# Kernel tuning notes

Measured on AMD Instinct MI355X. Metric: run time of the kernel, lower is better.

## Reference

```python
import jax, jax.numpy as jnp
import numpy as np

NCLS, NDF, B = 256, 512, 1024
ALP = 0.1


def setup_inputs() -> dict:
    key = jax.random.key(0)
    k1, k2, k3 = jax.random.split(key, 3)
    df = jax.random.normal(k1, (B, NDF), dtype=jnp.float32)
    gt = jax.random.randint(k2, (B,), 0, NCLS)
    fc = jax.random.normal(k3, (NCLS, NDF), dtype=jnp.float32)
    return {"df": df, "gt": gt, "fc": fc}


def _update_stats(df, gt):
    """Sequential per-sample running mean/var update (moving_avg=False branch).
    Faithful to the torch no_grad loop: per-class counter `it`, c1=it/(it+1),
    c2=1/(it+1); mean[t]=f when it==0 else mean[t]*c1+f*c2;
    var[t]=var[t]*c1 + (f-mean[t])**2 * c1*c2. Buffers start at zero.
    """
    mean0 = jnp.zeros((NCLS, NDF), jnp.float32)
    var0 = jnp.zeros((NCLS, NDF), jnp.float32)
    it0 = jnp.zeros((NCLS,), jnp.int32)

    def step(carry, xt):
        mean, var, it = carry
        f, t = xt
        n = it[t]
        nf = n.astype(jnp.float32)
        c1 = nf / (nf + 1.0)
        c2 = 1.0 / (nf + 1.0)
        m_t = jnp.where(n == 0, f, mean[t] * c1 + f * c2)
        a = (f - m_t) ** 2
        v_t = var[t] * c1 + a * c1 * c2
        return (mean.at[t].set(m_t), var.at[t].set(v_t), it.at[t].add(1)), None

    (mean, var, it), _ = jax.lax.scan(step, (mean0, var0, it0), (df, gt))
    return mean, var


def reference(df, gt, fc):
    # stats updated from detached features (torch uses no_grad)
    _, var = _update_stats(jax.lax.stop_gradient(df), gt)
    Var = var[gt]          # (B, ndf)
    Fc = fc[gt]            # (B, ndf): column of fc for each sample's class
    W = fc[None, :, :] - Fc[:, None, :]  # (B, ncls, ndf)
    # score[b,c] = W[b,c,:].df[b,:] + alp/2 * (W**2)[b,c,:].Var[b,:]
    score = jnp.einsum('bcd,bd->bc', W, df) \
        + 0.5 * ALP * jnp.einsum('bcd,bd->bc', W * W, Var)
    return score[:, :, None]  # (B, ncls, 1), matching torch matmul output
```

## Files before the change

kernel.cpp:

```cpp
#include <hip/hip_runtime.h>

#define NCLS 256
#define NDF  512
#define BSZ  1024
#define ALP  0.1f


typedef __attribute__((ext_vector_type(8))) short bf16x8;
typedef __attribute__((ext_vector_type(4))) float f32x4;

__device__ __forceinline__ unsigned rne_pk(float lo, float hi) {
    union { float f; unsigned u; } a, b;
    a.f = lo; b.f = hi;
    unsigned ua = (a.u + 0x7FFFu + ((a.u >> 16) & 1u)) >> 16;
    unsigned ub = (b.u + 0x7FFFu + ((b.u >> 16) & 1u)) & 0xFFFF0000u;
    return ua | ub;
}
__device__ __forceinline__ uint4 pk16(float4 p, float4 q) {
    uint4 r;
    r.x = rne_pk(p.x, p.y); r.y = rne_pk(p.z, p.w);
    r.z = rne_pk(q.x, q.y); r.w = rne_pk(q.z, q.w);
    return r;
}

__global__ __launch_bounds__(256) void fused_main(const float* __restrict__ df,
                                                  const int* __restrict__ gt,
                                                  const float* __restrict__ fc,
                                                  float* __restrict__ s1p,
                                                  float* __restrict__ Rp) {
    __shared__ union {
        struct { alignas(16) char A[64 * 128]; alignas(16) char B[64 * 128]; } g;
        struct { int gts[BSZ]; unsigned long long bmap[64 * 16]; } r;
    } sm;

    const int tid = threadIdx.x;
    const int bid = blockIdx.x;
    const int lane = tid & 63;
    const int wv = tid >> 6;
    const int wm = (wv >> 1) * 32, wn = (wv & 1) * 32;
    const int fr = lane & 15;
    const int fkb = (lane >> 4) * 16;
    const int fswz = (fr & 7) << 4;

    const int sr = tid >> 2;
    const int skb = (tid & 3) * 32;
    const int sswz = (sr & 7) << 4;

    f32x4 acc[2][2];
    acc[0][0] = 0.f; acc[0][1] = 0.f; acc[1][0] = 0.f; acc[1][1] = 0.f;

    auto mma_step = [&](int k0b) {
        const int kb = (k0b + fkb) ^ fswz;
        const bf16x8 aF0 = *(const bf16x8*)(sm.g.A + (wm + fr) * 128 + kb);
        const bf16x8 aF1 = *(const bf16x8*)(sm.g.A + (wm + 16 + fr) * 128 + kb);
        const bf16x8 bF0 = *(const bf16x8*)(sm.g.B + (wn + fr) * 128 + kb);
        const bf16x8 bF1 = *(const bf16x8*)(sm.g.B + (wn + 16 + fr) * 128 + kb);
        acc[0][0] = __builtin_amdgcn_mfma_f32_16x16x32_bf16(aF0, bF0, acc[0][0], 0, 0, 0);
        acc[0][1] = __builtin_amdgcn_mfma_f32_16x16x32_bf16(aF0, bF1, acc[0][1], 0, 0, 0);
        acc[1][0] = __builtin_amdgcn_mfma_f32_16x16x32_bf16(aF1, bF0, acc[1][0], 0, 0, 0);
        acc[1][1] = __builtin_amdgcn_mfma_f32_16x16x32_bf16(aF1, bF1, acc[1][1], 0, 0, 0);
    };
    auto store_tile = [&](float* base) {
#pragma unroll
        for (int mi = 0; mi < 2; ++mi)
#pragma unroll
            for (int ni = 0; ni < 2; ++ni)
#pragma unroll
                for (int r2 = 0; r2 < 4; ++r2)
                    base[(wm + mi * 16 + (lane >> 4) * 4 + r2) * NCLS + wn + ni * 16 + fr] =
                        acc[mi][ni][r2];
    };

    char* arow = sm.g.A + sr * 128;
    char* brow = sm.g.B + sr * 128;

    if (bid >= 128) {
        const int sid = bid - 128;
        const int z = sid & 7;
        const int tile = sid >> 3;
        const int bm = tile & 15, bn = tile >> 4;
        const float* Ag = df + (bm * 64 + sr) * NDF + z * 64 + (tid & 3) * 16;
        const float* Bg = fc + (bn * 64 + sr) * NDF + z * 64 + (tid & 3) * 16;

        const float4 a0 = ((const float4*)Ag)[0], a1 = ((const float4*)Ag)[1],
                     a2 = ((const float4*)Ag)[2], a3 = ((const float4*)Ag)[3];
        const float4 b0 = ((const float4*)Bg)[0], b1 = ((const float4*)Bg)[1],
                     b2 = ((const float4*)Bg)[2], b3 = ((const float4*)Bg)[3];
        *(uint4*)(arow + (skb ^ sswz)) = pk16(a0, a1);
        *(uint4*)(arow + ((skb + 16) ^ sswz)) = pk16(a2, a3);
        *(uint4*)(brow + (skb ^ sswz)) = pk16(b0, b1);
        *(uint4*)(brow + ((skb + 16) ^ sswz)) = pk16(b2, b3);
        __syncthreads();
        mma_step(0); mma_step(64);
        store_tile(s1p + z * (BSZ * NCLS) + (bm * 64) * NCLS + bn * 64);
    } else {
        const int z = bid & 7;
        const int tile = bid >> 3;
        const int bm = tile & 3, bn = tile >> 2;
        const int D0 = z * 64;
        const int clocal = sr;
        const int dg = tid & 3;
        const int myclass = bm * 64 + clocal;
        const int dim0 = D0 + dg * 16;

        const float* Bg = fc + (bn * 64 + sr) * NDF + D0 + (tid & 3) * 16;
        const float4 b0 = ((const float4*)Bg)[0], b1 = ((const float4*)Bg)[1],
                     b2 = ((const float4*)Bg)[2], b3 = ((const float4*)Bg)[3];

        for (int i = tid; i < BSZ; i += 256) sm.r.gts[i] = gt[i];
        for (int i = tid; i < 1024; i += 256) sm.r.bmap[i] = 0ull;
        __syncthreads();
        for (int i = tid; i < BSZ; i += 256) {
            const int c = sm.r.gts[i] - bm * 64;
            if ((unsigned)c < 64u) atomicOr(&sm.r.bmap[c * 16 + (i >> 6)], 1ull << (i & 63));
        }
        const float* fct = fc + myclass * NDF + dim0;
        float fcq[16];
        {
            const float4 q0 = ((const float4*)fct)[0], q1 = ((const float4*)fct)[1];
            const float4 q2 = ((const float4*)fct)[2], q3 = ((const float4*)fct)[3];
            fcq[0]=q0.x; fcq[1]=q0.y; fcq[2]=q0.z; fcq[3]=q0.w;
            fcq[4]=q1.x; fcq[5]=q1.y; fcq[6]=q1.z; fcq[7]=q1.w;
            fcq[8]=q2.x; fcq[9]=q2.y; fcq[10]=q2.z; fcq[11]=q2.w;
            fcq[12]=q3.x; fcq[13]=q3.y; fcq[14]=q3.z; fcq[15]=q3.w;
        }
        __syncthreads();

        float m[16], v[16];
#pragma unroll
        for (int j = 0; j < 16; ++j) { m[j] = 0.f; v[j] = 0.f; }
        float nf = 0.f;
        {
            int w = 0;
            unsigned long long bits = sm.r.bmap[clocal * 16];
            auto next = [&]() -> int {
                while (bits == 0ull) {
                    if (w >= 15) return -1;
                    bits = sm.r.bmap[clocal * 16 + (++w)];
                }
                const int b = __ffsll((unsigned long long)bits) - 1;
                bits &= bits - 1ull;
                return (w << 6) + b;
            };
            int cur = next();
            float f[16];
            if (cur >= 0) {
                const float* p = df + cur * NDF + dim0;
                const float4 q0 = ((const float4*)p)[0], q1 = ((const float4*)p)[1];
                const float4 q2 = ((const float4*)p)[2], q3 = ((const float4*)p)[3];
                f[0]=q0.x; f[1]=q0.y; f[2]=q0.z; f[3]=q0.w;
                f[4]=q1.x; f[5]=q1.y; f[6]=q1.z; f[7]=q1.w;
                f[8]=q2.x; f[9]=q2.y; f[10]=q2.z; f[11]=q2.w;
                f[12]=q3.x; f[13]=q3.y; f[14]=q3.z; f[15]=q3.w;
            }
            while (cur >= 0) {
                const int nxt = next();
                float g[16];
                if (nxt >= 0) {
                    const float* p = df + nxt * NDF + dim0;
                    const float4 q0 = ((const float4*)p)[0], q1 = ((const float4*)p)[1];
                    const float4 q2 = ((const float4*)p)[2], q3 = ((const float4*)p)[3];
                    g[0]=q0.x; g[1]=q0.y; g[2]=q0.z; g[3]=q0.w;
                    g[4]=q1.x; g[5]=q1.y; g[6]=q1.z; g[7]=q1.w;
                    g[8]=q2.x; g[9]=q2.y; g[10]=q2.z; g[11]=q2.w;
                    g[12]=q3.x; g[13]=q3.y; g[14]=q3.z; g[15]=q3.w;
                }
                const float c2 = 1.0f / (nf + 1.0f);
                const float c1 = nf * c2;
                const float c12 = c1 * c2;
#pragma unroll
                for (int j = 0; j < 16; ++j) {
                    m[j] = m[j] * c1 + f[j] * c2;
                    const float a = f[j] - m[j];
                    v[j] = v[j] * c1 + a * a * c12;
                }
                nf += 1.0f;
#pragma unroll
                for (int j = 0; j < 16; ++j) f[j] = g[j];
                cur = nxt;
            }
        }
        __syncthreads();

        {
            float4 p0, p1, p2, p3;
            p0.x=-2.f*fcq[0]*v[0];  p0.y=-2.f*fcq[1]*v[1];  p0.z=-2.f*fcq[2]*v[2];  p0.w=-2.f*fcq[3]*v[3];
            p1.x=-2.f*fcq[4]*v[4];  p1.y=-2.f*fcq[5]*v[5];  p1.z=-2.f*fcq[6]*v[6];  p1.w=-2.f*fcq[7]*v[7];
            p2.x=-2.f*fcq[8]*v[8];  p2.y=-2.f*fcq[9]*v[9];  p2.z=-2.f*fcq[10]*v[10]; p2.w=-2.f*fcq[11]*v[11];
            p3.x=-2.f*fcq[12]*v[12]; p3.y=-2.f*fcq[13]*v[13]; p3.z=-2.f*fcq[14]*v[14]; p3.w=-2.f*fcq[15]*v[15];
            *(uint4*)(arow + (skb ^ sswz)) = pk16(p0, p1);
            *(uint4*)(arow + ((skb + 16) ^ sswz)) = pk16(p2, p3);
            *(uint4*)(brow + (skb ^ sswz)) = pk16(b0, b1);
            *(uint4*)(brow + ((skb + 16) ^ sswz)) = pk16(b2, b3);
        }
        __syncthreads();
        mma_step(0); mma_step(64);
        __syncthreads();
        {
            float4 p0, p1, p2, p3, s0, s1, s2, s3;
            p0.x=v[0];  p0.y=v[1];  p0.z=v[2];  p0.w=v[3];
            p1.x=v[4];  p1.y=v[5];  p1.z=v[6];  p1.w=v[7];
            p2.x=v[8];  p2.y=v[9];  p2.z=v[10]; p2.w=v[11];
            p3.x=v[12]; p3.y=v[13]; p3.z=v[14]; p3.w=v[15];
            s0.x=b0.x*b0.x; s0.y=b0.y*b0.y; s0.z=b0.z*b0.z; s0.w=b0.w*b0.w;
            s1.x=b1.x*b1.x; s1.y=b1.y*b1.y; s1.z=b1.z*b1.z; s1.w=b1.w*b1.w;
            s2.x=b2.x*b2.x; s2.y=b2.y*b2.y; s2.z=b2.z*b2.z; s2.w=b2.w*b2.w;
            s3.x=b3.x*b3.x; s3.y=b3.y*b3.y; s3.z=b3.z*b3.z; s3.w=b3.w*b3.w;
            *(uint4*)(arow + (skb ^ sswz)) = pk16(p0, p1);
            *(uint4*)(arow + ((skb + 16) ^ sswz)) = pk16(p2, p3);
            *(uint4*)(brow + (skb ^ sswz)) = pk16(s0, s1);
            *(uint4*)(brow + ((skb + 16) ^ sswz)) = pk16(s2, s3);
        }
        __syncthreads();
        mma_step(0); mma_step(64);
        store_tile(Rp + z * (NCLS * NCLS) + (bm * 64) * NCLS + bn * 64);
    }
}

__global__ __launch_bounds__(256) void epilogue_kernel(const float* __restrict__ s1p,
                                                       const float* __restrict__ Rp,
                                                       const int* __restrict__ gt,
                                                       float* __restrict__ out) {
    const int b = blockIdx.x * 4 + (threadIdx.x >> 6);
    const int cq = (threadIdx.x & 63) * 4;
    const int t = gt[b];
    float4 v1 = make_float4(0.f, 0.f, 0.f, 0.f);
    float v1t = 0.f;
#pragma unroll
    for (int zz = 0; zz < 8; ++zz) {
        const float* row = s1p + zz * (BSZ * NCLS) + b * NCLS;
        const float4 q = *(const float4*)(row + cq);
        v1.x += q.x; v1.y += q.y; v1.z += q.z; v1.w += q.w;
        v1t += row[t];
    }
    float4 vR = make_float4(0.f, 0.f, 0.f, 0.f);
    float vRt = 0.f;
#pragma unroll
    for (int zz = 0; zz < 8; ++zz) {
        const float* row = Rp + zz * (NCLS * NCLS) + t * NCLS;
        const float4 q = *(const float4*)(row + cq);
        vR.x += q.x; vR.y += q.y; vR.z += q.z; vR.w += q.w;
        vRt += row[t];
    }
    float4 o;
    o.x = (v1.x - v1t) + 0.5f * ALP * (vR.x - vRt);
    o.y = (v1.y - v1t) + 0.5f * ALP * (vR.y - vRt);
    o.z = (v1.z - v1t) + 0.5f * ALP * (vR.z - vRt);
    o.w = (v1.w - v1t) + 0.5f * ALP * (vR.w - vRt);
    *(float4*)(out + b * NCLS + cq) = o;
}

extern "C" void kernel_launch(void* const* d_in, const int* in_sizes, int n_in,
                              void* d_out, int out_size, void* d_ws, size_t ws_size,
                              hipStream_t stream) {
    const float* df = (const float*)d_in[0];
    const int* gt = (const int*)d_in[1];
    const float* fc = (const float*)d_in[2];
    float* out = (float*)d_out;

    float* ws = (float*)d_ws;
    float* s1p = ws;
    float* Rp = s1p + 8 * BSZ * NCLS;

    fused_main<<<640, 256, 0, stream>>>(df, gt, fc, s1p, Rp);
    epilogue_kernel<<<256, 256, 0, stream>>>(s1p, Rp, gt, out);
}
```

Measured before the change: 27.25 us.

## Halve split-K partials for GEMM blocks and fuse the two R-path MFMAs into one K=128 pass

The df·fc GEMM blocks now cover 128 of K each instead of 64, giving 4 split-K slices instead of 8. That halves the s1 partial buffers the epilogue writes and reads, and drops the launch from 640 to 384 blocks. In the stats/R blocks, the two chained MFMA passes (-2·fc·var times fc, and var times fc²) are concatenated along K into one 256-byte-wide shared tile, removing a sync and a reload round. The cost is more registers per thread, double the shared memory, and fewer blocks for latency hiding.

```diff
diff --git a/kernel.cpp b/kernel.cpp
--- a/kernel.cpp
+++ b/kernel.cpp
@@ -29,7 +29,7 @@
                                                   float* __restrict__ s1p,
                                                   float* __restrict__ Rp) {
     __shared__ union {
-        struct { alignas(16) char A[64 * 128]; alignas(16) char B[64 * 128]; } g;
+        struct { alignas(16) char A[64 * 256]; alignas(16) char B[64 * 256]; } g;
         struct { int gts[BSZ]; unsigned long long bmap[64 * 16]; } r;
     } sm;
 
@@ -43,18 +43,19 @@
     const int fswz = (fr & 7) << 4;
 
     const int sr = tid >> 2;
-    const int skb = (tid & 3) * 32;
     const int sswz = (sr & 7) << 4;
+    char* arow = sm.g.A + sr * 256;
+    char* brow = sm.g.B + sr * 256;
 
     f32x4 acc[2][2];
     acc[0][0] = 0.f; acc[0][1] = 0.f; acc[1][0] = 0.f; acc[1][1] = 0.f;
 
     auto mma_step = [&](int k0b) {
         const int kb = (k0b + fkb) ^ fswz;
-        const bf16x8 aF0 = *(const bf16x8*)(sm.g.A + (wm + fr) * 128 + kb);
-        const bf16x8 aF1 = *(const bf16x8*)(sm.g.A + (wm + 16 + fr) * 128 + kb);
-        const bf16x8 bF0 = *(const bf16x8*)(sm.g.B + (wn + fr) * 128 + kb);
-        const bf16x8 bF1 = *(const bf16x8*)(sm.g.B + (wn + 16 + fr) * 128 + kb);
+        const bf16x8 aF0 = *(const bf16x8*)(sm.g.A + (wm + fr) * 256 + kb);
+        const bf16x8 aF1 = *(const bf16x8*)(sm.g.A + (wm + 16 + fr) * 256 + kb);
+        const bf16x8 bF0 = *(const bf16x8*)(sm.g.B + (wn + fr) * 256 + kb);
+        const bf16x8 bF1 = *(const bf16x8*)(sm.g.B + (wn + 16 + fr) * 256 + kb);
         acc[0][0] = __builtin_amdgcn_mfma_f32_16x16x32_bf16(aF0, bF0, acc[0][0], 0, 0, 0);
         acc[0][1] = __builtin_amdgcn_mfma_f32_16x16x32_bf16(aF0, bF1, acc[0][1], 0, 0, 0);
         acc[1][0] = __builtin_amdgcn_mfma_f32_16x16x32_bf16(aF1, bF0, acc[1][0], 0, 0, 0);
@@ -71,27 +72,30 @@
                         acc[mi][ni][r2];
     };
 
-    char* arow = sm.g.A + sr * 128;
-    char* brow = sm.g.B + sr * 128;
-
     if (bid >= 128) {
         const int sid = bid - 128;
-        const int z = sid & 7;
-        const int tile = sid >> 3;
+        const int z = sid & 3;
+        const int tile = sid >> 2;
         const int bm = tile & 15, bn = tile >> 4;
-        const float* Ag = df + (bm * 64 + sr) * NDF + z * 64 + (tid & 3) * 16;
-        const float* Bg = fc + (bn * 64 + sr) * NDF + z * 64 + (tid & 3) * 16;
-
-        const float4 a0 = ((const float4*)Ag)[0], a1 = ((const float4*)Ag)[1],
-                     a2 = ((const float4*)Ag)[2], a3 = ((const float4*)Ag)[3];
-        const float4 b0 = ((const float4*)Bg)[0], b1 = ((const float4*)Bg)[1],
-                     b2 = ((const float4*)Bg)[2], b3 = ((const float4*)Bg)[3];
-        *(uint4*)(arow + (skb ^ sswz)) = pk16(a0, a1);
-        *(uint4*)(arow + ((skb + 16) ^ sswz)) = pk16(a2, a3);
-        *(uint4*)(brow + (skb ^ sswz)) = pk16(b0, b1);
-        *(uint4*)(brow + ((skb + 16) ^ sswz)) = pk16(b2, b3);
-        __syncthreads();
-        mma_step(0); mma_step(64);
+        const float* Ag = df + (bm * 64 + sr) * NDF + z * 128 + (tid & 3) * 32;
+        const float* Bg = fc + (bn * 64 + sr) * NDF + z * 128 + (tid & 3) * 32;
+        const int kbase = (tid & 3) * 64;
+
+        float4 a[8], b[8];
+#pragma unroll
+        for (int i = 0; i < 8; ++i) a[i] = ((const float4*)Ag)[i];
+#pragma unroll
+        for (int i = 0; i < 8; ++i) b[i] = ((const float4*)Bg)[i];
+        *(uint4*)(arow + ((kbase + 0) ^ sswz)) = pk16(a[0], a[1]);
+        *(uint4*)(arow + ((kbase + 16) ^ sswz)) = pk16(a[2], a[3]);
+        *(uint4*)(arow + ((kbase + 32) ^ sswz)) = pk16(a[4], a[5]);
+        *(uint4*)(arow + ((kbase + 48) ^ sswz)) = pk16(a[6], a[7]);
+        *(uint4*)(brow + ((kbase + 0) ^ sswz)) = pk16(b[0], b[1]);
+        *(uint4*)(brow + ((kbase + 16) ^ sswz)) = pk16(b[2], b[3]);
+        *(uint4*)(brow + ((kbase + 32) ^ sswz)) = pk16(b[4], b[5]);
+        *(uint4*)(brow + ((kbase + 48) ^ sswz)) = pk16(b[6], b[7]);
+        __syncthreads();
+        mma_step(0); mma_step(64); mma_step(128); mma_step(192);
         store_tile(s1p + z * (BSZ * NCLS) + (bm * 64) * NCLS + bn * 64);
     } else {
         const int z = bid & 7;
@@ -99,11 +103,12 @@
         const int bm = tile & 3, bn = tile >> 2;
         const int D0 = z * 64;
         const int clocal = sr;
-        const int dg = tid & 3;
         const int myclass = bm * 64 + clocal;
-        const int dim0 = D0 + dg * 16;
-
-        const float* Bg = fc + (bn * 64 + sr) * NDF + D0 + (tid & 3) * 16;
+        const int dim0 = D0 + (tid & 3) * 16;
+        const int kbl = (tid & 3) * 32;
+        const int kbq = 128 + kbl;
+
+        const float* Bg = fc + (bn * 64 + sr) * NDF + dim0;
         const float4 b0 = ((const float4*)Bg)[0], b1 = ((const float4*)Bg)[1],
                      b2 = ((const float4*)Bg)[2], b3 = ((const float4*)Bg)[3];
 
@@ -183,36 +188,32 @@
         __syncthreads();
 
         {
+            float4 l0, l1, l2, l3;
+            l0.x=-2.f*fcq[0]*v[0];  l0.y=-2.f*fcq[1]*v[1];  l0.z=-2.f*fcq[2]*v[2];  l0.w=-2.f*fcq[3]*v[3];
+            l1.x=-2.f*fcq[4]*v[4];  l1.y=-2.f*fcq[5]*v[5];  l1.z=-2.f*fcq[6]*v[6];  l1.w=-2.f*fcq[7]*v[7];
+            l2.x=-2.f*fcq[8]*v[8];  l2.y=-2.f*fcq[9]*v[9];  l2.z=-2.f*fcq[10]*v[10]; l2.w=-2.f*fcq[11]*v[11];
+            l3.x=-2.f*fcq[12]*v[12]; l3.y=-2.f*fcq[13]*v[13]; l3.z=-2.f*fcq[14]*v[14]; l3.w=-2.f*fcq[15]*v[15];
             float4 p0, p1, p2, p3;
-            p0.x=-2.f*fcq[0]*v[0];  p0.y=-2.f*fcq[1]*v[1];  p0.z=-2.f*fcq[2]*v[2];  p0.w=-2.f*fcq[3]*v[3];
-            p1.x=-2.f*fcq[4]*v[4];  p1.y=-2.f*fcq[5]*v[5];  p1.z=-2.f*fcq[6]*v[6];  p1.w=-2.f*fcq[7]*v[7];
-            p2.x=-2.f*fcq[8]*v[8];  p2.y=-2.f*fcq[9]*v[9];  p2.z=-2.f*fcq[10]*v[10]; p2.w=-2.f*fcq[11]*v[11];
-            p3.x=-2.f*fcq[12]*v[12]; p3.y=-2.f*fcq[13]*v[13]; p3.z=-2.f*fcq[14]*v[14]; p3.w=-2.f*fcq[15]*v[15];
-            *(uint4*)(arow + (skb ^ sswz)) = pk16(p0, p1);
-            *(uint4*)(arow + ((skb + 16) ^ sswz)) = pk16(p2, p3);
-            *(uint4*)(brow + (skb ^ sswz)) = pk16(b0, b1);
-            *(uint4*)(brow + ((skb + 16) ^ sswz)) = pk16(b2, b3);
-        }
-        __syncthreads();
-        mma_step(0); mma_step(64);
-        __syncthreads();
-        {
-            float4 p0, p1, p2, p3, s0, s1, s2, s3;
             p0.x=v[0];  p0.y=v[1];  p0.z=v[2];  p0.w=v[3];
             p1.x=v[4];  p1.y=v[5];  p1.z=v[6];  p1.w=v[7];
             p2.x=v[8];  p2.y=v[9];  p2.z=v[10]; p2.w=v[11];
             p3.x=v[12]; p3.y=v[13]; p3.z=v[14]; p3.w=v[15];
+            float4 s0, s1, s2, s3;
             s0.x=b0.x*b0.x; s0.y=b0.y*b0.y; s0.z=b0.z*b0.z; s0.w=b0.w*b0.w;
             s1.x=b1.x*b1.x; s1.y=b1.y*b1.y; s1.z=b1.z*b1.z; s1.w=b1.w*b1.w;
             s2.x=b2.x*b2.x; s2.y=b2.y*b2.y; s2.z=b2.z*b2.z; s2.w=b2.w*b2.w;
             s3.x=b3.x*b3.x; s3.y=b3.y*b3.y; s3.z=b3.z*b3.z; s3.w=b3.w*b3.w;
-            *(uint4*)(arow + (skb ^ sswz)) = pk16(p0, p1);
-            *(uint4*)(arow + ((skb + 16) ^ sswz)) = pk16(p2, p3);
-            *(uint4*)(brow + (skb ^ sswz)) = pk16(s0, s1);
-            *(uint4*)(brow + ((skb + 16) ^ sswz)) = pk16(s2, s3);
-        }
-        __syncthreads();
-        mma_step(0); mma_step(64);
+            *(uint4*)(arow + ((kbl + 0) ^ sswz)) = pk16(l0, l1);
+            *(uint4*)(arow + ((kbl + 16) ^ sswz)) = pk16(l2, l3);
+            *(uint4*)(arow + ((kbq + 0) ^ sswz)) = pk16(p0, p1);
+            *(uint4*)(arow + ((kbq + 16) ^ sswz)) = pk16(p2, p3);
+            *(uint4*)(brow + ((kbl + 0) ^ sswz)) = pk16(b0, b1);
+            *(uint4*)(brow + ((kbl + 16) ^ sswz)) = pk16(b2, b3);
+            *(uint4*)(brow + ((kbq + 0) ^ sswz)) = pk16(s0, s1);
+            *(uint4*)(brow + ((kbq + 16) ^ sswz)) = pk16(s2, s3);
+        }
+        __syncthreads();
+        mma_step(0); mma_step(64); mma_step(128); mma_step(192);
         store_tile(Rp + z * (NCLS * NCLS) + (bm * 64) * NCLS + bn * 64);
     }
 }
@@ -227,7 +228,7 @@
     float4 v1 = make_float4(0.f, 0.f, 0.f, 0.f);
     float v1t = 0.f;
 #pragma unroll
-    for (int zz = 0; zz < 8; ++zz) {
+    for (int zz = 0; zz < 4; ++zz) {
         const float* row = s1p + zz * (BSZ * NCLS) + b * NCLS;
         const float4 q = *(const float4*)(row + cq);
         v1.x += q.x; v1.y += q.y; v1.z += q.z; v1.w += q.w;
@@ -260,8 +261,8 @@
 
     float* ws = (float*)d_ws;
     float* s1p = ws;
-    float* Rp = s1p + 8 * BSZ * NCLS;
-
-    fused_main<<<640, 256, 0, stream>>>(df, gt, fc, s1p, Rp);
+    float* Rp = s1p + 4 * BSZ * NCLS;
+
+    fused_main<<<384, 256, 0, stream>>>(df, gt, fc, s1p, Rp);
     epilogue_kernel<<<256, 256, 0, stream>>>(s1p, Rp, gt, out);
 }
```

Result: faster. 25.92 us (-4.9%).
